# Kernel tuning notes

Measured on AMD Instinct MI355X. Metric: run time of the kernel, lower is better.

The kernel has to match this reference:

```python
import jax, jax.numpy as jnp
import numpy as np

B, S, H = 2, 8192, 1024
NUM_HEADS = 16
HEAD_DIM = H // NUM_HEADS
KERNEL = 7
DILATION = 1
SCALE = 1.0 / np.sqrt(HEAD_DIM)


def setup_inputs() -> dict:
    key = jax.random.key(0)
    ks = jax.random.split(key, 9)
    init = 0.02
    return {
        "hidden_states": jax.random.normal(ks[0], (B, S, H), dtype=jnp.float32),
        "w_q": jax.random.normal(ks[1], (H, H), dtype=jnp.float32) * init,
        "b_q": jnp.zeros((H,), dtype=jnp.float32),
        "w_k": jax.random.normal(ks[2], (H, H), dtype=jnp.float32) * init,
        "b_k": jnp.zeros((H,), dtype=jnp.float32),
        "w_v": jax.random.normal(ks[3], (H, H), dtype=jnp.float32) * init,
        "b_v": jnp.zeros((H,), dtype=jnp.float32),
        "w_o": jax.random.normal(ks[4], (H, H), dtype=jnp.float32) * init,
        "b_o": jnp.zeros((H,), dtype=jnp.float32),
    }


def reference(hidden_states, w_q, b_q, w_k, b_k, w_v, b_v, w_o, b_o):
    b, s, h = hidden_states.shape
    # QKV projections (weights stored [in, out])
    q = hidden_states @ w_q + b_q
    k = hidden_states @ w_k + b_k
    v = hidden_states @ w_v + b_v
    # [B, nH, S, hd]
    q = q.reshape(b, s, NUM_HEADS, HEAD_DIM).transpose(0, 2, 1, 3)
    k = k.reshape(b, s, NUM_HEADS, HEAD_DIM).transpose(0, 2, 1, 3)
    v = v.reshape(b, s, NUM_HEADS, HEAD_DIM).transpose(0, 2, 1, 3)

    # Neighborhood window indices: for query i, keys at i + (j - K//2)*dilation
    offsets = (jnp.arange(KERNEL) - KERNEL // 2) * DILATION  # [K]
    idx = jnp.arange(s)[:, None] + offsets[None, :]          # [S, K]
    valid = (idx >= 0) & (idx < s)                           # [S, K]
    idx_c = jnp.clip(idx, 0, s - 1)

    k_win = k[:, :, idx_c, :]  # [B, nH, S, K, hd]
    v_win = v[:, :, idx_c, :]  # [B, nH, S, K, hd]

    scores = jnp.einsum('bhsd,bhskd->bhsk', q, k_win) * SCALE
    scores = jnp.where(valid[None, None], scores, -jnp.inf)
    attn = jax.nn.softmax(scores, axis=-1)                   # [B, nH, S, K]
    out = jnp.einsum('bhsk,bhskd->bhsd', attn, v_win)        # [B, nH, S, hd]

    out = out.transpose(0, 2, 1, 3).reshape(b, s, h)
    return out @ w_o + b_o
```

## Files before the change

kernel.cpp:

```cpp
#include <hip/hip_runtime.h>


typedef __bf16 bf16x8 __attribute__((ext_vector_type(8)));
typedef float f32x4 __attribute__((ext_vector_type(4)));
typedef int int4v __attribute__((ext_vector_type(4)));
typedef unsigned short u16x8 __attribute__((ext_vector_type(8)));
typedef __attribute__((address_space(1))) void as1_void;
typedef __attribute__((address_space(3))) void as3_void;

__device__ __forceinline__ float bf2f(unsigned short u) {
    union { unsigned int u; float f; } c;
    c.u = ((unsigned int)u) << 16;
    return c.f;
}
__device__ __forceinline__ unsigned short f2bf(float f) {
    union { float f; unsigned int u; } c;
    c.f = f;
    unsigned int u = c.u;
    u += 0x7fffu + ((u >> 16) & 1u);
    return (unsigned short)(u >> 16);
}

__global__ __launch_bounds__(256) void prep(
    const float* __restrict__ X, const float* __restrict__ w0,
    const float* __restrict__ w1, const float* __restrict__ w2,
    const float* __restrict__ w3, const float* __restrict__ bq,
    const float* __restrict__ bk, const float* __restrict__ bv,
    unsigned short* __restrict__ Xb, unsigned short* __restrict__ t0,
    unsigned short* __restrict__ t3, float* __restrict__ biasQ) {
    __shared__ unsigned short tile[32][33];
    const int bid = blockIdx.x;
    if (bid < 16384) {
        int i = bid * 256 + threadIdx.x;
        float4 v = ((const float4*)X)[i];
        ushort4 o;
        o.x = f2bf(v.x); o.y = f2bf(v.y); o.z = f2bf(v.z); o.w = f2bf(v.w);
        ((ushort4*)Xb)[i] = o;
    } else if (bid < 20480) {
        const int t = bid - 16384;
        const int z = t >> 10;
        const int rem = t & 1023;
        const float* W = (z == 0) ? w0 : (z == 1) ? w1 : (z == 2) ? w2 : w3;
        unsigned short* Wt = (z == 3) ? t3 : t0 + (size_t)z * 1048576;
        const int c0 = (rem & 31) * 32;
        const int r0 = (rem >> 5) * 32;
        const int tx = threadIdx.x & 31;
        const int ty = threadIdx.x >> 5;
#pragma unroll
        for (int i = 0; i < 32; i += 8)
            tile[ty + i][tx] = f2bf(W[(size_t)(r0 + ty + i) * 1024 + c0 + tx]);
        __syncthreads();
#pragma unroll
        for (int i = 0; i < 32; i += 8)
            Wt[(size_t)(c0 + ty + i) * 1024 + r0 + tx] = tile[tx][ty + i];
    } else {
        int i = (bid - 20480) * 256 + threadIdx.x;
        if (i < 3072)
            biasQ[i] = (i < 1024) ? bq[i] : ((i < 2048) ? bk[i - 1024] : bv[i - 2048]);
    }
}

__global__ __launch_bounds__(512, 2) void gemm_qkv8(
    const unsigned short* __restrict__ A, const unsigned short* __restrict__ Bt,
    const float* __restrict__ bias, unsigned short* __restrict__ Cb) {
    constexpr int K = 1024;
    constexpr int NT = 16;
    __shared__ unsigned short smem[65536];
    const int tid  = threadIdx.x;
    const int lane = tid & 63;
    const int wave = tid >> 6;
    const int quad = lane >> 4;
    const int mr   = lane & 15;

    const int id  = blockIdx.x;
    const int swz = (id & 7) * 96 + (id >> 3);
    const int bm  = (swz / 12) * 256;
    const int bn  = (swz % 12) * 256;
    const int wm  = (wave >> 2) * 128;
    const int wn  = (wave & 3) * 64;

    const int r0 = tid >> 3;
    const int g8 = ((lane & 7) ^ ((lane >> 3) & 7)) * 8;
    const unsigned short* srcA = A  + (size_t)(bm + r0) * K + g8;
    const unsigned short* srcB = Bt + (size_t)(bn + r0) * K + g8;

    auto stage = [&](const unsigned short* gb, int ldsByte, int kt) {
#pragma unroll
        for (int l = 0; l < 2; ++l)
            __builtin_amdgcn_global_load_lds(
                (const as1_void*)(gb + (size_t)l * 65536 + kt),
                (as3_void*)((char*)smem + ldsByte + l * 8192 + tid * 16),
                16, 0, 0);
    };

    stage(srcA,          0,     0);
    stage(srcA + 131072, 16384, 0);
    stage(srcB,          32768, 0);
    stage(srcB + 131072, 49152, 0);
    stage(srcB,          65536 + 32768, 64);
    stage(srcB + 131072, 65536 + 49152, 64);
    asm volatile("s_waitcnt vmcnt(4)" ::: "memory");
    asm volatile("s_barrier" ::: "memory");

    const int aRow = (wm + mr) * 64;
    const int bRow = 16384 + (wn + mr) * 64;
    const int c8_0 = ((0 * 4 + quad) ^ (mr & 7)) * 8;
    const int c8_1 = ((1 * 4 + quad) ^ (mr & 7)) * 8;

    f32x4 acc[8][4] = {};

    for (int t = 0; t < NT; ++t) {
        const int bufS  = (t & 1) << 15;
        const int nbufB = ((t + 1) & 1) << 16;
        const int cbufB = (t & 1) << 16;
        const int ktA = (t + 1 < NT ? t + 1 : NT - 1) * 64;
        const int ktB = (t + 2 < NT ? t + 2 : NT - 1) * 64;

        bf16x8 afL[4][2], bA[2][2], bB[2][2];
#pragma unroll
        for (int i = 0; i < 4; ++i) {
            afL[i][0] = *(const bf16x8*)(smem + bufS + aRow + i * 1024 + c8_0);
            afL[i][1] = *(const bf16x8*)(smem + bufS + aRow + i * 1024 + c8_1);
        }
#pragma unroll
        for (int j = 0; j < 2; ++j) {
            bA[j][0] = *(const bf16x8*)(smem + bufS + bRow + j * 1024 + c8_0);
            bA[j][1] = *(const bf16x8*)(smem + bufS + bRow + j * 1024 + c8_1);
        }
#pragma unroll
        for (int j = 0; j < 2; ++j) {
            bB[j][0] = *(const bf16x8*)(smem + bufS + bRow + (j + 2) * 1024 + c8_0);
            bB[j][1] = *(const bf16x8*)(smem + bufS + bRow + (j + 2) * 1024 + c8_1);
        }
        stage(srcA, nbufB, ktA);
        __builtin_amdgcn_s_setprio(1);
#pragma unroll
        for (int i = 0; i < 4; ++i)
#pragma unroll
            for (int j = 0; j < 2; ++j) {
                acc[i][j] = __builtin_amdgcn_mfma_f32_16x16x32_bf16(afL[i][0], bA[j][0], acc[i][j], 0, 0, 0);
                acc[i][j] = __builtin_amdgcn_mfma_f32_16x16x32_bf16(afL[i][1], bA[j][1], acc[i][j], 0, 0, 0);
            }
        __builtin_amdgcn_s_setprio(0);
        asm volatile("s_barrier" ::: "memory");

        stage(srcA + 131072, nbufB + 16384, ktA);
        __builtin_amdgcn_s_setprio(1);
#pragma unroll
        for (int i = 0; i < 4; ++i)
#pragma unroll
            for (int j = 0; j < 2; ++j) {
                acc[i][j + 2] = __builtin_amdgcn_mfma_f32_16x16x32_bf16(afL[i][0], bB[j][0], acc[i][j + 2], 0, 0, 0);
                acc[i][j + 2] = __builtin_amdgcn_mfma_f32_16x16x32_bf16(afL[i][1], bB[j][1], acc[i][j + 2], 0, 0, 0);
            }
        __builtin_amdgcn_s_setprio(0);
        asm volatile("s_barrier" ::: "memory");

        bf16x8 afH[4][2];
#pragma unroll
        for (int i = 0; i < 4; ++i) {
            afH[i][0] = *(const bf16x8*)(smem + bufS + aRow + (i + 4) * 1024 + c8_0);
            afH[i][1] = *(const bf16x8*)(smem + bufS + aRow + (i + 4) * 1024 + c8_1);
        }
        stage(srcB, cbufB + 32768, ktB);
        __builtin_amdgcn_s_setprio(1);
#pragma unroll
        for (int i = 0; i < 4; ++i)
#pragma unroll
            for (int j = 0; j < 2; ++j) {
                acc[i + 4][j + 2] = __builtin_amdgcn_mfma_f32_16x16x32_bf16(afH[i][0], bB[j][0], acc[i + 4][j + 2], 0, 0, 0);
                acc[i + 4][j + 2] = __builtin_amdgcn_mfma_f32_16x16x32_bf16(afH[i][1], bB[j][1], acc[i + 4][j + 2], 0, 0, 0);
            }
        __builtin_amdgcn_s_setprio(0);
        asm volatile("s_barrier" ::: "memory");

        stage(srcB + 131072, cbufB + 49152, ktB);
        __builtin_amdgcn_s_setprio(1);
#pragma unroll
        for (int i = 0; i < 4; ++i)
#pragma unroll
            for (int j = 0; j < 2; ++j) {
                acc[i + 4][j] = __builtin_amdgcn_mfma_f32_16x16x32_bf16(afH[i][0], bA[j][0], acc[i + 4][j], 0, 0, 0);
                acc[i + 4][j] = __builtin_amdgcn_mfma_f32_16x16x32_bf16(afH[i][1], bA[j][1], acc[i + 4][j], 0, 0, 0);
            }
        __builtin_amdgcn_s_setprio(0);
        asm volatile("s_waitcnt vmcnt(4)" ::: "memory");
        asm volatile("s_barrier" ::: "memory");
    }

    asm volatile("s_waitcnt vmcnt(0) lgkmcnt(0)" ::: "memory");
    asm volatile("s_barrier" ::: "memory");

    unsigned short* ep = smem + wave * 8192;
#pragma unroll
    for (int h = 0; h < 2; ++h) {
#pragma unroll
        for (int j = 0; j < 4; ++j) {
            const float bvv = bias[bn + wn + j * 16 + mr];
#pragma unroll
            for (int i = 0; i < 4; ++i)
#pragma unroll
                for (int r = 0; r < 4; ++r)
                    ep[(i * 16 + quad * 4 + r) * 68 + j * 16 + mr] =
                        f2bf(acc[h * 4 + i][j][r] + bvv);
        }
#pragma unroll
        for (int p = 0; p < 8; ++p) {
            const int row = p * 8 + (lane >> 3);
            const int gr = lane & 7;
            int4v v = *(const int4v*)(ep + row * 68 + gr * 8);
            *(int4v*)(Cb + (size_t)(bm + wm + h * 64 + row) * 3072 + bn + wn + gr * 8) = v;
        }
    }
}

__global__ __launch_bounds__(256) void attn_wave4(
    const unsigned short* __restrict__ QKV, unsigned short* __restrict__ out) {
    const int lane = threadIdx.x & 63;
    const int wv   = threadIdx.x >> 6;
    const int id   = blockIdx.x;
    const int swz  = (id & 7) * 128 + (id >> 3);
    const int tok0 = swz * 16 + wv * 4;
    const int s0   = tok0 & 8191;
    const int bb   = tok0 - s0;
    const int le8  = lane * 8;

    const float NEG = -__builtin_inff();

    u16x8 qa[4][2];
#pragma unroll
    for (int t = 0; t < 4; ++t) {
        const size_t rq = (size_t)(tok0 + t) * 3072;
        qa[t][0] = *(const u16x8*)(QKV + rq + le8);
        qa[t][1] = *(const u16x8*)(QKV + rq + 512 + le8);
    }

    float sc0[4][7], sc1[4][7];
#pragma unroll
    for (int ri = 0; ri < 10; ++ri) {
        const int ks = s0 + ri - 3;
        const bool okr = (ks >= 0) & (ks < 8192);
        const int kc = ks < 0 ? 0 : (ks > 8191 ? 8191 : ks);
        const size_t kb = (size_t)(bb + kc) * 3072 + 1024;
        u16x8 k0 = *(const u16x8*)(QKV + kb + le8);
        u16x8 k1 = *(const u16x8*)(QKV + kb + 512 + le8);
#pragma unroll
        for (int t = 0; t < 4; ++t) {
            const int j = ri - t;
            if (j >= 0 && j < 7) {
                float d0 = 0.f, d1 = 0.f;
#pragma unroll
                for (int e = 0; e < 8; ++e) {
                    d0 += bf2f(qa[t][0][e]) * bf2f(k0[e]);
                    d1 += bf2f(qa[t][1][e]) * bf2f(k1[e]);
                }
#pragma unroll
                for (int off = 1; off <= 4; off <<= 1) {
                    d0 += __shfl_xor(d0, off);
                    d1 += __shfl_xor(d1, off);
                }
                sc0[t][j] = okr ? d0 * 0.125f : NEG;
                sc1[t][j] = okr ? d1 * 0.125f : NEG;
            }
        }
    }

    float w0[4][7], w1[4][7];
#pragma unroll
    for (int t = 0; t < 4; ++t) {
        float mx0 = sc0[t][0], mx1 = sc1[t][0];
#pragma unroll
        for (int j = 1; j < 7; ++j) { mx0 = fmaxf(mx0, sc0[t][j]); mx1 = fmaxf(mx1, sc1[t][j]); }
        float s0s = 0.f, s1s = 0.f;
#pragma unroll
        for (int j = 0; j < 7; ++j) {
            w0[t][j] = __builtin_amdgcn_exp2f((sc0[t][j] - mx0) * 1.44269504f);
            w1[t][j] = __builtin_amdgcn_exp2f((sc1[t][j] - mx1) * 1.44269504f);
            s0s += w0[t][j]; s1s += w1[t][j];
        }
        const float i0 = __builtin_amdgcn_rcpf(s0s);
        const float i1 = __builtin_amdgcn_rcpf(s1s);
#pragma unroll
        for (int j = 0; j < 7; ++j) { w0[t][j] *= i0; w1[t][j] *= i1; }
    }

    float o0[4][8] = {}, o1[4][8] = {};
#pragma unroll
    for (int ri = 0; ri < 10; ++ri) {
        const int ks = s0 + ri - 3;
        const int kc = ks < 0 ? 0 : (ks > 8191 ? 8191 : ks);
        const size_t vb = (size_t)(bb + kc) * 3072 + 2048;
        u16x8 v0 = *(const u16x8*)(QKV + vb + le8);
        u16x8 v1 = *(const u16x8*)(QKV + vb + 512 + le8);
        float vf0[8], vf1[8];
#pragma unroll
        for (int e = 0; e < 8; ++e) { vf0[e] = bf2f(v0[e]); vf1[e] = bf2f(v1[e]); }
#pragma unroll
        for (int t = 0; t < 4; ++t) {
            const int j = ri - t;
            if (j >= 0 && j < 7) {
#pragma unroll
                for (int e = 0; e < 8; ++e) {
                    o0[t][e] += w0[t][j] * vf0[e];
                    o1[t][e] += w1[t][j] * vf1[e];
                }
            }
        }
    }

#pragma unroll
    for (int t = 0; t < 4; ++t) {
        const size_t dst = (size_t)(tok0 + t) * 1024;
        u16x8 a, b2;
#pragma unroll
        for (int e = 0; e < 8; ++e) { a[e] = f2bf(o0[t][e]); b2[e] = f2bf(o1[t][e]); }
        *(u16x8*)(out + dst + le8) = a;
        *(u16x8*)(out + dst + 512 + le8) = b2;
    }
}

template <int MODE, int MT>
__device__ __forceinline__ void gemm_body(
    const unsigned short* __restrict__ A, const unsigned short* __restrict__ Bt,
    const float* __restrict__ bias, float* __restrict__ Cf,
    int N, int K) {
    __shared__ unsigned short smem[MT * 2048 + 8192];
    const int tid = threadIdx.x;
    const int lane = tid & 63;
    const int wave = tid >> 6;
    const int bm = blockIdx.y * (MT * 32);
    const int bn = blockIdx.x * 128;
    const int wm = (wave >> 1) * (MT * 16);
    const int wn = (wave & 1) * 64;
    const int quad = lane >> 4;
    const int mr = lane & 15;

    const unsigned short* gA[MT];
    const unsigned short* gB[4];
    char* lA[MT];
    char* lB[4];
#pragma unroll
    for (int k = 0; k < MT; ++k) {
        const int q = (k * 4 + wave) * 64 + lane;
        const int row = q >> 3;
        const int c8 = (q & 7) ^ (row & 7);
        gA[k] = A + (size_t)(bm + row) * K + c8 * 8;
        lA[k] = (char*)smem + (size_t)(k * 4 + wave) * 1024;
    }
#pragma unroll
    for (int k = 0; k < 4; ++k) {
        const int q = (k * 4 + wave) * 64 + lane;
        const int row = q >> 3;
        const int c8 = (q & 7) ^ (row & 7);
        gB[k] = Bt + (size_t)(bn + row) * K + c8 * 8;
        lB[k] = (char*)smem + (size_t)MT * 4096 + (size_t)(k * 4 + wave) * 1024;
    }

    f32x4 acc[MT][4] = {};

    for (int kt = 0; kt < K; kt += 64) {
#pragma unroll
        for (int k = 0; k < MT; ++k) {
            __builtin_amdgcn_global_load_lds((as1_void*)gA[k], (as3_void*)lA[k], 16, 0, 0);
            gA[k] += 64;
        }
#pragma unroll
        for (int k = 0; k < 4; ++k) {
            __builtin_amdgcn_global_load_lds((as1_void*)gB[k], (as3_void*)lB[k], 16, 0, 0);
            gB[k] += 64;
        }
        __syncthreads();

#pragma unroll
        for (int kk = 0; kk < 2; ++kk) {
            const int c8 = (kk * 4 + quad) ^ (mr & 7);
            bf16x8 af[MT], bfr[4];
#pragma unroll
            for (int i = 0; i < MT; ++i)
                af[i] = *(const bf16x8*)(smem + (wm + i * 16 + mr) * 64 + c8 * 8);
#pragma unroll
            for (int j = 0; j < 4; ++j)
                bfr[j] = *(const bf16x8*)(smem + MT * 2048 + (wn + j * 16 + mr) * 64 + c8 * 8);
#pragma unroll
            for (int i = 0; i < MT; ++i)
#pragma unroll
                for (int j = 0; j < 4; ++j)
                    acc[i][j] = __builtin_amdgcn_mfma_f32_16x16x32_bf16(
                        af[i], bfr[j], acc[i][j], 0, 0, 0);
        }
        __syncthreads();
    }

    if (MODE == 0) {
        float* epf = (float*)smem + wave * 1280;
#pragma unroll
        for (int j = 0; j < 4; ++j) {
            const int gcol0 = bn + wn + j * 16;
            const float bv = bias[gcol0 + mr];
#pragma unroll
            for (int h2 = 0; h2 < MT / 4; ++h2) {
#pragma unroll
                for (int i2 = 0; i2 < 4; ++i2)
#pragma unroll
                    for (int r = 0; r < 4; ++r)
                        epf[(i2 * 16 + quad * 4 + r) * 20 + mr] = acc[h2 * 4 + i2][j][r] + bv;
#pragma unroll
                for (int p = 0; p < 4; ++p) {
                    const int dr = p * 16 + (lane >> 2);
                    const int ch = lane & 3;
                    f32x4 v = *(const f32x4*)(epf + dr * 20 + ch * 4);
                    *(f32x4*)(Cf + (size_t)(bm + wm + h2 * 64 + dr) * N + gcol0 + ch * 4) = v;
                }
            }
        }
    }
}

__global__ __launch_bounds__(256, 4) void gemm_out(
    const unsigned short* __restrict__ A, const unsigned short* __restrict__ Bt,
    const float* __restrict__ bias, float* __restrict__ Cf, int N, int K) {
    gemm_body<0, 4>(A, Bt, bias, Cf, N, K);
}

extern "C" void kernel_launch(void* const* d_in, const int* in_sizes, int n_in,
                              void* d_out, int out_size, void* d_ws, size_t ws_size,
                              hipStream_t stream) {
    (void)in_sizes; (void)n_in; (void)out_size; (void)ws_size;
    const float* X  = (const float*)d_in[0];
    const float* wq = (const float*)d_in[1];
    const float* bq = (const float*)d_in[2];
    const float* wk = (const float*)d_in[3];
    const float* bk = (const float*)d_in[4];
    const float* wv = (const float*)d_in[5];
    const float* bv = (const float*)d_in[6];
    const float* wo = (const float*)d_in[7];
    const float* bo = (const float*)d_in[8];
    float* out = (float*)d_out;

    char* ws = (char*)d_ws;
    unsigned short* Xb    = (unsigned short*)(ws);
    unsigned short* WtQKV = (unsigned short*)(ws + 33554432);
    unsigned short* WtO   = (unsigned short*)(ws + 39845888);
    unsigned short* QKV   = (unsigned short*)(ws + 41943040);
    unsigned short* AttnO = (unsigned short*)(ws + 142606336);
    float*          biasQ = (float*)(ws + 176160768);

    prep<<<20492, 256, 0, stream>>>(X, wq, wk, wv, wo, bq, bk, bv,
                                    Xb, WtQKV, WtO, biasQ);

    gemm_qkv8<<<768, 512, 0, stream>>>(Xb, WtQKV, biasQ, QKV);

    attn_wave4<<<1024, 256, 0, stream>>>(QKV, AttnO);

    gemm_out<<<dim3(8, 128), 256, 0, stream>>>(AttnO, WtO, bo, out, 1024, 1024);
}
```

Before: 327.7 us.

## Replace output GEMM with 256x256 pipelined 8-wave kernel and merge QKV staging barriers

Replaces the simple 128x128 single-buffered output-projection GEMM with a 256x256 tile, 512-thread kernel modelled on the QKV GEMM: it prefetches into double-buffered LDS with direct global-to-LDS loads, raises MFMA priority with setprio, and swizzles block order across XCDs. It also issues both halves of each staging step together in the QKV GEMM and in the new kernel, dropping one barrier per half-iteration. The larger tiles give more reuse per load and overlap loads with compute, at the cost of only 256 blocks (about one wave of work on the chip) and a riskier barrier/buffer ordering once the intermediate barriers are removed.

```diff
diff --git a/kernel.cpp b/kernel.cpp
--- a/kernel.cpp
+++ b/kernel.cpp
@@ -133,6 +133,7 @@
             bB[j][1] = *(const bf16x8*)(smem + bufS + bRow + (j + 2) * 1024 + c8_1);
         }
         stage(srcA, nbufB, ktA);
+        stage(srcA + 131072, nbufB + 16384, ktA);
         __builtin_amdgcn_s_setprio(1);
 #pragma unroll
         for (int i = 0; i < 4; ++i)
@@ -141,11 +142,6 @@
                 acc[i][j] = __builtin_amdgcn_mfma_f32_16x16x32_bf16(afL[i][0], bA[j][0], acc[i][j], 0, 0, 0);
                 acc[i][j] = __builtin_amdgcn_mfma_f32_16x16x32_bf16(afL[i][1], bA[j][1], acc[i][j], 0, 0, 0);
             }
-        __builtin_amdgcn_s_setprio(0);
-        asm volatile("s_barrier" ::: "memory");
-
-        stage(srcA + 131072, nbufB + 16384, ktA);
-        __builtin_amdgcn_s_setprio(1);
 #pragma unroll
         for (int i = 0; i < 4; ++i)
 #pragma unroll
@@ -163,6 +159,7 @@
             afH[i][1] = *(const bf16x8*)(smem + bufS + aRow + (i + 4) * 1024 + c8_1);
         }
         stage(srcB, cbufB + 32768, ktB);
+        stage(srcB + 131072, cbufB + 49152, ktB);
         __builtin_amdgcn_s_setprio(1);
 #pragma unroll
         for (int i = 0; i < 4; ++i)
@@ -171,11 +168,6 @@
                 acc[i + 4][j + 2] = __builtin_amdgcn_mfma_f32_16x16x32_bf16(afH[i][0], bB[j][0], acc[i + 4][j + 2], 0, 0, 0);
                 acc[i + 4][j + 2] = __builtin_amdgcn_mfma_f32_16x16x32_bf16(afH[i][1], bB[j][1], acc[i + 4][j + 2], 0, 0, 0);
             }
-        __builtin_amdgcn_s_setprio(0);
-        asm volatile("s_barrier" ::: "memory");
-
-        stage(srcB + 131072, cbufB + 49152, ktB);
-        __builtin_amdgcn_s_setprio(1);
 #pragma unroll
         for (int i = 0; i < 4; ++i)
 #pragma unroll
@@ -210,6 +202,152 @@
             const int gr = lane & 7;
             int4v v = *(const int4v*)(ep + row * 68 + gr * 8);
             *(int4v*)(Cb + (size_t)(bm + wm + h * 64 + row) * 3072 + bn + wn + gr * 8) = v;
+        }
+    }
+}
+
+__global__ __launch_bounds__(512, 2) void gemm_out8(
+    const unsigned short* __restrict__ A, const unsigned short* __restrict__ Bt,
+    const float* __restrict__ bias, float* __restrict__ Cf) {
+    constexpr int K = 1024;
+    constexpr int NT = 16;
+    __shared__ unsigned short smem[65536];
+    const int tid  = threadIdx.x;
+    const int lane = tid & 63;
+    const int wave = tid >> 6;
+    const int quad = lane >> 4;
+    const int mr   = lane & 15;
+
+    const int id  = blockIdx.x;
+    const int swz = (id & 7) * 32 + (id >> 3);
+    const int bm  = (swz >> 2) * 256;
+    const int bn  = (swz & 3) * 256;
+    const int wm  = (wave >> 2) * 128;
+    const int wn  = (wave & 3) * 64;
+
+    const int r0 = tid >> 3;
+    const int g8 = ((lane & 7) ^ ((lane >> 3) & 7)) * 8;
+    const unsigned short* srcA = A  + (size_t)(bm + r0) * K + g8;
+    const unsigned short* srcB = Bt + (size_t)(bn + r0) * K + g8;
+
+    auto stage = [&](const unsigned short* gb, int ldsByte, int kt) {
+#pragma unroll
+        for (int l = 0; l < 2; ++l)
+            __builtin_amdgcn_global_load_lds(
+                (const as1_void*)(gb + (size_t)l * 65536 + kt),
+                (as3_void*)((char*)smem + ldsByte + l * 8192 + tid * 16),
+                16, 0, 0);
+    };
+
+    stage(srcA,          0,     0);
+    stage(srcA + 131072, 16384, 0);
+    stage(srcB,          32768, 0);
+    stage(srcB + 131072, 49152, 0);
+    stage(srcB,          65536 + 32768, 64);
+    stage(srcB + 131072, 65536 + 49152, 64);
+    asm volatile("s_waitcnt vmcnt(4)" ::: "memory");
+    asm volatile("s_barrier" ::: "memory");
+
+    const int aRow = (wm + mr) * 64;
+    const int bRow = 16384 + (wn + mr) * 64;
+    const int c8_0 = ((0 * 4 + quad) ^ (mr & 7)) * 8;
+    const int c8_1 = ((1 * 4 + quad) ^ (mr & 7)) * 8;
+
+    f32x4 acc[8][4] = {};
+
+    for (int t = 0; t < NT; ++t) {
+        const int bufS  = (t & 1) << 15;
+        const int nbufB = ((t + 1) & 1) << 16;
+        const int cbufB = (t & 1) << 16;
+        const int ktA = (t + 1 < NT ? t + 1 : NT - 1) * 64;
+        const int ktB = (t + 2 < NT ? t + 2 : NT - 1) * 64;
+
+        bf16x8 afL[4][2], bA[2][2], bB[2][2];
+#pragma unroll
+        for (int i = 0; i < 4; ++i) {
+            afL[i][0] = *(const bf16x8*)(smem + bufS + aRow + i * 1024 + c8_0);
+            afL[i][1] = *(const bf16x8*)(smem + bufS + aRow + i * 1024 + c8_1);
+        }
+#pragma unroll
+        for (int j = 0; j < 2; ++j) {
+            bA[j][0] = *(const bf16x8*)(smem + bufS + bRow + j * 1024 + c8_0);
+            bA[j][1] = *(const bf16x8*)(smem + bufS + bRow + j * 1024 + c8_1);
+        }
+#pragma unroll
+        for (int j = 0; j < 2; ++j) {
+            bB[j][0] = *(const bf16x8*)(smem + bufS + bRow + (j + 2) * 1024 + c8_0);
+            bB[j][1] = *(const bf16x8*)(smem + bufS + bRow + (j + 2) * 1024 + c8_1);
+        }
+        stage(srcA, nbufB, ktA);
+        stage(srcA + 131072, nbufB + 16384, ktA);
+        __builtin_amdgcn_s_setprio(1);
+#pragma unroll
+        for (int i = 0; i < 4; ++i)
+#pragma unroll
+            for (int j = 0; j < 2; ++j) {
+                acc[i][j] = __builtin_amdgcn_mfma_f32_16x16x32_bf16(afL[i][0], bA[j][0], acc[i][j], 0, 0, 0);
+                acc[i][j] = __builtin_amdgcn_mfma_f32_16x16x32_bf16(afL[i][1], bA[j][1], acc[i][j], 0, 0, 0);
+            }
+#pragma unroll
+        for (int i = 0; i < 4; ++i)
+#pragma unroll
+            for (int j = 0; j < 2; ++j) {
+                acc[i][j + 2] = __builtin_amdgcn_mfma_f32_16x16x32_bf16(afL[i][0], bB[j][0], acc[i][j + 2], 0, 0, 0);
+                acc[i][j + 2] = __builtin_amdgcn_mfma_f32_16x16x32_bf16(afL[i][1], bB[j][1], acc[i][j + 2], 0, 0, 0);
+            }
+        __builtin_amdgcn_s_setprio(0);
+        asm volatile("s_barrier" ::: "memory");
+
+        bf16x8 afH[4][2];
+#pragma unroll
+        for (int i = 0; i < 4; ++i) {
+            afH[i][0] = *(const bf16x8*)(smem + bufS + aRow + (i + 4) * 1024 + c8_0);
+            afH[i][1] = *(const bf16x8*)(smem + bufS + aRow + (i + 4) * 1024 + c8_1);
+        }
+        stage(srcB, cbufB + 32768, ktB);
+        stage(srcB + 131072, cbufB + 49152, ktB);
+        __builtin_amdgcn_s_setprio(1);
+#pragma unroll
+        for (int i = 0; i < 4; ++i)
+#pragma unroll
+            for (int j = 0; j < 2; ++j) {
+                acc[i + 4][j + 2] = __builtin_amdgcn_mfma_f32_16x16x32_bf16(afH[i][0], bB[j][0], acc[i + 4][j + 2], 0, 0, 0);
+                acc[i + 4][j + 2] = __builtin_amdgcn_mfma_f32_16x16x32_bf16(afH[i][1], bB[j][1], acc[i + 4][j + 2], 0, 0, 0);
+            }
+#pragma unroll
+        for (int i = 0; i < 4; ++i)
+#pragma unroll
+            for (int j = 0; j < 2; ++j) {
+                acc[i + 4][j] = __builtin_amdgcn_mfma_f32_16x16x32_bf16(afH[i][0], bA[j][0], acc[i + 4][j], 0, 0, 0);
+                acc[i + 4][j] = __builtin_amdgcn_mfma_f32_16x16x32_bf16(afH[i][1], bA[j][1], acc[i + 4][j], 0, 0, 0);
+            }
+        __builtin_amdgcn_s_setprio(0);
+        asm volatile("s_waitcnt vmcnt(4)" ::: "memory");
+        asm volatile("s_barrier" ::: "memory");
+    }
+
+    asm volatile("s_waitcnt vmcnt(0) lgkmcnt(0)" ::: "memory");
+    asm volatile("s_barrier" ::: "memory");
+
+    float* epf = (float*)((char*)smem + wave * 16384);
+#pragma unroll
+    for (int hh = 0; hh < 4; ++hh) {
+#pragma unroll
+        for (int j = 0; j < 4; ++j) {
+            const float bvv = bias[bn + wn + j * 16 + mr];
+#pragma unroll
+            for (int i2 = 0; i2 < 2; ++i2)
+#pragma unroll
+                for (int r = 0; r < 4; ++r)
+                    epf[(i2 * 16 + quad * 4 + r) * 68 + j * 16 + mr] =
+                        acc[hh * 2 + i2][j][r] + bvv;
+        }
+#pragma unroll
+        for (int p = 0; p < 8; ++p) {
+            const int row = p * 4 + (lane >> 4);
+            const int ch = lane & 15;
+            f32x4 v = *(const f32x4*)(epf + row * 68 + ch * 4);
+            *(f32x4*)(Cf + (size_t)(bm + wm + hh * 32 + row) * 1024 + bn + wn + ch * 4) = v;
         }
     }
 }
@@ -317,109 +455,6 @@
         *(u16x8*)(out + dst + le8) = a;
         *(u16x8*)(out + dst + 512 + le8) = b2;
     }
-}
-
-template <int MODE, int MT>
-__device__ __forceinline__ void gemm_body(
-    const unsigned short* __restrict__ A, const unsigned short* __restrict__ Bt,
-    const float* __restrict__ bias, float* __restrict__ Cf,
-    int N, int K) {
-    __shared__ unsigned short smem[MT * 2048 + 8192];
-    const int tid = threadIdx.x;
-    const int lane = tid & 63;
-    const int wave = tid >> 6;
-    const int bm = blockIdx.y * (MT * 32);
-    const int bn = blockIdx.x * 128;
-    const int wm = (wave >> 1) * (MT * 16);
-    const int wn = (wave & 1) * 64;
-    const int quad = lane >> 4;
-    const int mr = lane & 15;
-
-    const unsigned short* gA[MT];
-    const unsigned short* gB[4];
-    char* lA[MT];
-    char* lB[4];
-#pragma unroll
-    for (int k = 0; k < MT; ++k) {
-        const int q = (k * 4 + wave) * 64 + lane;
-        const int row = q >> 3;
-        const int c8 = (q & 7) ^ (row & 7);
-        gA[k] = A + (size_t)(bm + row) * K + c8 * 8;
-        lA[k] = (char*)smem + (size_t)(k * 4 + wave) * 1024;
-    }
-#pragma unroll
-    for (int k = 0; k < 4; ++k) {
-        const int q = (k * 4 + wave) * 64 + lane;
-        const int row = q >> 3;
-        const int c8 = (q & 7) ^ (row & 7);
-        gB[k] = Bt + (size_t)(bn + row) * K + c8 * 8;
-        lB[k] = (char*)smem + (size_t)MT * 4096 + (size_t)(k * 4 + wave) * 1024;
-    }
-
-    f32x4 acc[MT][4] = {};
-
-    for (int kt = 0; kt < K; kt += 64) {
-#pragma unroll
-        for (int k = 0; k < MT; ++k) {
-            __builtin_amdgcn_global_load_lds((as1_void*)gA[k], (as3_void*)lA[k], 16, 0, 0);
-            gA[k] += 64;
-        }
-#pragma unroll
-        for (int k = 0; k < 4; ++k) {
-            __builtin_amdgcn_global_load_lds((as1_void*)gB[k], (as3_void*)lB[k], 16, 0, 0);
-            gB[k] += 64;
-        }
-        __syncthreads();
-
-#pragma unroll
-        for (int kk = 0; kk < 2; ++kk) {
-            const int c8 = (kk * 4 + quad) ^ (mr & 7);
-            bf16x8 af[MT], bfr[4];
-#pragma unroll
-            for (int i = 0; i < MT; ++i)
-                af[i] = *(const bf16x8*)(smem + (wm + i * 16 + mr) * 64 + c8 * 8);
-#pragma unroll
-            for (int j = 0; j < 4; ++j)
-                bfr[j] = *(const bf16x8*)(smem + MT * 2048 + (wn + j * 16 + mr) * 64 + c8 * 8);
-#pragma unroll
-            for (int i = 0; i < MT; ++i)
-#pragma unroll
-                for (int j = 0; j < 4; ++j)
-                    acc[i][j] = __builtin_amdgcn_mfma_f32_16x16x32_bf16(
-                        af[i], bfr[j], acc[i][j], 0, 0, 0);
-        }
-        __syncthreads();
-    }
-
-    if (MODE == 0) {
-        float* epf = (float*)smem + wave * 1280;
-#pragma unroll
-        for (int j = 0; j < 4; ++j) {
-            const int gcol0 = bn + wn + j * 16;
-            const float bv = bias[gcol0 + mr];
-#pragma unroll
-            for (int h2 = 0; h2 < MT / 4; ++h2) {
-#pragma unroll
-                for (int i2 = 0; i2 < 4; ++i2)
-#pragma unroll
-                    for (int r = 0; r < 4; ++r)
-                        epf[(i2 * 16 + quad * 4 + r) * 20 + mr] = acc[h2 * 4 + i2][j][r] + bv;
-#pragma unroll
-                for (int p = 0; p < 4; ++p) {
-                    const int dr = p * 16 + (lane >> 2);
-                    const int ch = lane & 3;
-                    f32x4 v = *(const f32x4*)(epf + dr * 20 + ch * 4);
-                    *(f32x4*)(Cf + (size_t)(bm + wm + h2 * 64 + dr) * N + gcol0 + ch * 4) = v;
-                }
-            }
-        }
-    }
-}
-
-__global__ __launch_bounds__(256, 4) void gemm_out(
-    const unsigned short* __restrict__ A, const unsigned short* __restrict__ Bt,
-    const float* __restrict__ bias, float* __restrict__ Cf, int N, int K) {
-    gemm_body<0, 4>(A, Bt, bias, Cf, N, K);
 }
 
 extern "C" void kernel_launch(void* const* d_in, const int* in_sizes, int n_in,
@@ -452,5 +487,5 @@
 
     attn_wave4<<<1024, 256, 0, stream>>>(QKV, AttnO);
 
-    gemm_out<<<dim3(8, 128), 256, 0, stream>>>(AttnO, WtO, bo, out, 1024, 1024);
-}
+    gemm_out8<<<256, 512, 0, stream>>>(AttnO, WtO, bo, out);
+}
```

Result: faster. 310.9 us (median of 2 runs) (-5.1%).
